# Optimization experiments

Hardware: AMD Instinct MI355X
Metric: run time of the kernel (lower is better)

The kernel has to match this reference:

```python
import jax, jax.numpy as jnp
import numpy as np
from jax import lax

N, K, F = 512, 512, 96
DM = 256   # hidden_dim == d_model
DS = 256   # d_state (must equal d_model for the original code to run)
L = 2      # num_layers
EPS = 1e-5


def layer_norm(x, g, b):
    mu = jnp.mean(x, axis=-1, keepdims=True)
    var = jnp.var(x, axis=-1, keepdims=True)
    return (x - mu) * jax.lax.rsqrt(var + EPS) * g + b


def setup_inputs() -> dict:
    key = jax.random.key(0)
    ks = jax.random.split(key, 20)
    n = lambda k, shape, s=0.02: jax.random.normal(k, shape, dtype=jnp.float32) * s
    inp = {
        "x": jax.random.normal(ks[0], (N, K, F), dtype=jnp.float32),
        # input_proj
        "in_w": n(ks[1], (DM, F), 0.05), "in_b": jnp.zeros((DM,), jnp.float32),
        "in_ln_g": jnp.ones((DM,), jnp.float32), "in_ln_b": jnp.zeros((DM,), jnp.float32),
        # per-layer Mamba params, stacked on leading L axis
        "ln_g": jnp.ones((L, DM), jnp.float32), "ln_b": jnp.zeros((L, DM), jnp.float32),
        "gate_w": n(ks[2], (L, DM, DM), 0.05), "gate_b": jnp.zeros((L, DM), jnp.float32),
        "sp_w": n(ks[3], (L, DS, DM), 0.05), "sp_b": jnp.zeros((L, DS), jnp.float32),
        "op_w": n(ks[4], (L, DM, DM), 0.05), "op_b": jnp.zeros((L, DM), jnp.float32),
        "A_log": n(ks[5], (L, DM, DS), 0.02),
        "D": jnp.ones((L, DM), jnp.float32),
        # output_proj
        "out_w": n(ks[6], (DM, DM), 0.05), "out_b": jnp.zeros((DM,), jnp.float32),
        "out_ln_g": jnp.ones((DM,), jnp.float32), "out_ln_b": jnp.zeros((DM,), jnp.float32),
    }
    return inp


def _ssm_scan(state0, decay, s):
    # state_t = decay * state_{t-1} + s_t ; s: [N, K, DS]
    def step(st, s_t):
        st = st * decay + s_t
        return st, st
    state, states = lax.scan(step, state0, jnp.swapaxes(s, 0, 1))
    return state, jnp.swapaxes(states, 0, 1)  # [N, K, DS]


def reference(x, in_w, in_b, in_ln_g, in_ln_b, ln_g, ln_b, gate_w, gate_b,
              sp_w, sp_b, op_w, op_b, A_log, D, out_w, out_b, out_ln_g, out_ln_b):
    # input_proj: Linear -> LayerNorm -> GELU
    h = jnp.einsum('nkf,df->nkd', x, in_w) + in_b
    h = jax.nn.gelu(layer_norm(h, in_ln_g, in_ln_b), approximate=False)

    state = jnp.zeros((x.shape[0], DS), dtype=h.dtype)
    for l in range(L):
        res = h
        z = layer_norm(h, ln_g[l], ln_b[l])
        xg = jax.nn.silu(jnp.einsum('nkd,ed->nke', z, gate_w[l]) + gate_b[l])
        s = jnp.einsum('nkd,sd->nks', xg, sp_w[l]) + sp_b[l]          # state_proj
        decay = jnp.exp(-jnp.mean(jnp.exp(A_log[l]), axis=-1))         # exp(mean(A)), A=-exp(A_log)
        state, states = _ssm_scan(state, decay, s)
        y = jnp.einsum('nks,sd->nkd', states, sp_w[l]) + D[l] * xg     # matmul(state, W_sp) + D*u
        h = jnp.einsum('nkd,ed->nke', y, op_w[l]) + op_b[l] + res      # out_proj + residual

    pooled = h[:, -1, :]                                               # pooling='last'
    out = jnp.einsum('nd,ed->ne', pooled, out_w) + out_b
    out = jax.nn.gelu(layer_norm(out, out_ln_g, out_ln_b), approximate=False)
    return out
```

## Files before the change

kernel.cpp:

```cpp
#include <hip/hip_runtime.h>
#include <hip/hip_bf16.h>


typedef __attribute__((ext_vector_type(8))) __bf16 bf16x8;
typedef __attribute__((ext_vector_type(8))) short short8;
typedef __attribute__((ext_vector_type(4))) float f32x4;
typedef __attribute__((ext_vector_type(4))) unsigned u32x4;

#define NSEQ 512
#define KSEQ 512
#define FIN 96
#define DMODEL 256
#define MTOT (NSEQ*KSEQ)

__device__ __forceinline__ unsigned short f2bf(float f){
  union { float f; unsigned u; } v; v.f = f;
  unsigned r = (v.u + 0x7FFFu + ((v.u >> 16) & 1u)) >> 16;
  return (unsigned short)r;
}
__device__ __forceinline__ float bf2f(unsigned short b){
  union { unsigned u; float f; } v; v.u = ((unsigned)b) << 16; return v.f;
}
__device__ __forceinline__ unsigned pk_bf16(float lo, float hi){
  unsigned r;
  asm("v_cvt_pk_bf16_f32 %0, %1, %2" : "=v"(r) : "v"(lo), "v"(hi));
  return r;
}
__device__ __forceinline__ float gelu_f(float x){
  return 0.5f * x * (1.0f + erff(x * 0.70710678118654752440f));
}
__device__ __forceinline__ float silu_f(float x){
  return x / (1.0f + __expf(-x));
}
__device__ __forceinline__ unsigned swzA(int row, int kbyte){
  return ((unsigned)(row*512 + kbyte)) ^ (unsigned)((row & 7) << 4);
}
__device__ __forceinline__ unsigned swzB(int n, int kbyte){
  return ((unsigned)(n*128 + kbyte)) ^ (unsigned)((n & 7) << 4);
}

__device__ __forceinline__ void gemm_w8(const unsigned short* __restrict__ wb,
                                        const char* As, f32x4 (&acc)[4][2],
                                        int lane, int c0)
{
  const int lr  = lane & 15;
  const int lk8 = (lane >> 4) * 8;
  const unsigned short* bp = wb + (size_t)(c0 + lr)*256 + lk8;
  bf16x8 bb[4][2];
  #pragma unroll
  for(int p = 0; p < 4; ++p)
    #pragma unroll
    for(int fc = 0; fc < 2; ++fc)
      bb[p][fc] = *(const bf16x8*)(bp + fc*4096 + p*32);
  #pragma unroll
  for(int kc = 0; kc < 8; ++kc){
    bf16x8 af[4];
    #pragma unroll
    for(int fr = 0; fr < 4; ++fr)
      af[fr] = *(const bf16x8*)(As + swzA(fr*16 + lr, kc*64 + lk8*2));
    #pragma unroll
    for(int fr = 0; fr < 4; ++fr)
      #pragma unroll
      for(int fc = 0; fc < 2; ++fc)
        acc[fr][fc] = __builtin_amdgcn_mfma_f32_16x16x32_bf16(af[fr], bb[kc&3][fc], acc[fr][fc], 0, 0, 0);
    if(kc < 4){
      #pragma unroll
      for(int fc = 0; fc < 2; ++fc)
        bb[kc&3][fc] = *(const bf16x8*)(bp + fc*4096 + (kc+4)*32);
    }
  }
}

__device__ __forceinline__ void zero_acc2(f32x4 (&acc)[4][2]){
  #pragma unroll
  for(int a=0;a<4;++a)
    #pragma unroll
    for(int b=0;b<2;++b)
      acc[a][b] = (f32x4){0.f,0.f,0.f,0.f};
}
__device__ __forceinline__ void zero_acc(f32x4 (&acc)[4][4]){
  #pragma unroll
  for(int a=0;a<4;++a)
    #pragma unroll
    for(int b=0;b<4;++b)
      acc[a][b] = (f32x4){0.f,0.f,0.f,0.f};
}

template<int KCH>
__device__ __forceinline__ void gemm_64x256(const unsigned short* __restrict__ wb,
                                            char* As, char* Bs,
                                            f32x4 (&acc)[4][4], int tid)
{
  const int lane = tid & 63;
  const int c0   = (tid >> 6) * 64;
  const int lr   = lane & 15;
  const int lk16 = (lane >> 4) * 16;
  #pragma unroll
  for(int kc = 0; kc < KCH; ++kc){
    __syncthreads();
    {
      const unsigned short* src = wb + (size_t)tid * (KCH*64) + kc*64;
      #pragma unroll
      for(int i = 0; i < 8; ++i){
        short8 v = *(const short8*)(src + i*8);
        *(short8*)(Bs + swzB(tid, i*16)) = v;
      }
    }
    __syncthreads();
    #pragma unroll
    for(int t2 = 0; t2 < 2; ++t2){
      bf16x8 af[4], bfr[4];
      #pragma unroll
      for(int fr = 0; fr < 4; ++fr)
        af[fr] = *(const bf16x8*)(As + swzA(fr*16 + lr, kc*128 + t2*64 + lk16));
      #pragma unroll
      for(int fc = 0; fc < 4; ++fc)
        bfr[fc] = *(const bf16x8*)(Bs + swzB(c0 + fc*16 + lr, t2*64 + lk16));
      #pragma unroll
      for(int fr = 0; fr < 4; ++fr)
        #pragma unroll
        for(int fc = 0; fc < 4; ++fc)
          acc[fr][fc] = __builtin_amdgcn_mfma_f32_16x16x32_bf16(af[fr], bfr[fc], acc[fr][fc], 0, 0, 0);
    }
  }
}

__global__ void k_cvt(const float* __restrict__ s, unsigned short* __restrict__ d, int n){
  int i = blockIdx.x*256 + threadIdx.x;
  if(i < n) d[i] = f2bf(s[i]);
}
__global__ void k_cvt_inw(const float* __restrict__ w, unsigned short* __restrict__ d){
  int i = blockIdx.x*256 + threadIdx.x;
  int n = i >> 7, f = i & 127;
  d[i] = (f < 96) ? f2bf(w[n*96 + f]) : (unsigned short)0;
}
__global__ void k_spT(const float* __restrict__ spw, unsigned short* __restrict__ d){
  int l = blockIdx.y;
  int i = blockIdx.x*256 + threadIdx.x;
  int dd = i >> 8, ss = i & 255;
  d[l*65536 + i] = f2bf(spw[l*65536 + ss*256 + dd]);
}
__global__ void k_decay(const float* __restrict__ A_log, float* __restrict__ decay){
  __shared__ float red[4];
  const int b = blockIdx.x;
  const int tid = threadIdx.x;
  float v = expf(A_log[(size_t)b*256 + tid]);
  #pragma unroll
  for(int o = 32; o >= 1; o >>= 1) v += __shfl_xor(v, o);
  if((tid & 63) == 0) red[tid >> 6] = v;
  __syncthreads();
  if(tid == 0){
    float s = red[0] + red[1] + red[2] + red[3];
    decay[b] = expf(-s * (1.f/256.f));
  }
}

__global__ __launch_bounds__(256) void k_in_proj(
    const float* __restrict__ x_g,
    const unsigned short* __restrict__ in_wb,
    const float* __restrict__ in_b,
    const float* __restrict__ ln_gv, const float* __restrict__ ln_bv,
    unsigned short* __restrict__ h_g)
{
  __shared__ char smem[65536];
  char* As = smem; char* Bs = smem + 32768;
  const int tid = threadIdx.x;
  const int m0 = blockIdx.x * 64;
  const int lane = tid & 63, c0w = (tid>>6)*64, lr = lane & 15, rb = (lane>>4)*4;
  {
    const int r = tid >> 2, cq = tid & 3;
    const float* src = x_g + (size_t)(m0 + r)*FIN + cq*24;
    unsigned short tmp[24] __attribute__((aligned(16)));
    #pragma unroll
    for(int i = 0; i < 6; ++i){
      float4 v = *(const float4*)(src + i*4);
      tmp[4*i]=f2bf(v.x); tmp[4*i+1]=f2bf(v.y); tmp[4*i+2]=f2bf(v.z); tmp[4*i+3]=f2bf(v.w);
    }
    #pragma unroll
    for(int i = 0; i < 3; ++i)
      *(short8*)(As + swzA(r, cq*48 + i*16)) = *(const short8*)(tmp + i*8);
    if(cq == 3){
      short8 z8 = {0,0,0,0,0,0,0,0};
      #pragma unroll
      for(int i = 0; i < 4; ++i)
        *(short8*)(As + swzA(r, 192 + i*16)) = z8;
    }
  }
  f32x4 acc[4][4]; zero_acc(acc);
  gemm_64x256<2>(in_wb, As, Bs, acc, tid);
  __syncthreads();
  #pragma unroll
  for(int fc = 0; fc < 4; ++fc){
    const int col = c0w + fc*16 + lr;
    const float bb = in_b[col];
    #pragma unroll
    for(int fr = 0; fr < 4; ++fr)
      #pragma unroll
      for(int rg = 0; rg < 4; ++rg){
        const int row = fr*16 + rb + rg;
        *(float*)(smem + (((unsigned)(row*1024 + col*4)) ^ ((row&7)<<4))) = acc[fr][fc][rg] + bb;
      }
  }
  __syncthreads();
  {
    const int r = tid >> 2, c0 = (tid & 3) * 64;
    float vals[64]; float sm = 0.f, sq = 0.f;
    #pragma unroll
    for(int i = 0; i < 16; ++i){
      float4 v = *(const float4*)(smem + (((unsigned)(r*1024 + (c0 + i*4)*4)) ^ ((r&7)<<4)));
      vals[4*i]=v.x; vals[4*i+1]=v.y; vals[4*i+2]=v.z; vals[4*i+3]=v.w;
    }
    #pragma unroll
    for(int i = 0; i < 64; ++i){ sm += vals[i]; sq += vals[i]*vals[i]; }
    sm += __shfl_xor(sm, 1); sm += __shfl_xor(sm, 2);
    sq += __shfl_xor(sq, 1); sq += __shfl_xor(sq, 2);
    const float mu = sm * (1.f/256.f);
    const float rstd = rsqrtf(sq * (1.f/256.f) - mu*mu + 1e-5f);
    unsigned short* dst = h_g + (size_t)(m0 + r)*DMODEL + c0;
    #pragma unroll
    for(int i = 0; i < 8; ++i){
      float g[8];
      #pragma unroll
      for(int j = 0; j < 8; ++j){
        const int c = c0 + i*8 + j;
        g[j] = gelu_f((vals[i*8+j]-mu)*rstd*ln_gv[c] + ln_bv[c]);
      }
      u32x4 o;
      o[0] = pk_bf16(g[0],g[1]); o[1] = pk_bf16(g[2],g[3]);
      o[2] = pk_bf16(g[4],g[5]); o[3] = pk_bf16(g[6],g[7]);
      *(u32x4*)(dst + i*8) = o;
    }
  }
}

__global__ __launch_bounds__(512,2) void k_layers(
    unsigned short* __restrict__ h_g,
    const unsigned short* __restrict__ gate_w0,
    const unsigned short* __restrict__ sp_w0,
    const unsigned short* __restrict__ spT_w0,
    const unsigned short* __restrict__ op_w0,
    const float* __restrict__ ln_g0, const float* __restrict__ ln_b0,
    const float* __restrict__ gate_b0, const float* __restrict__ sp_b0,
    const float* __restrict__ decay0, const float* __restrict__ D0,
    const float* __restrict__ op_b0)
{
  __shared__ char As[32768];
  __shared__ char Ss[32768];
  const int tid = threadIdx.x;
  const int n = blockIdx.x;
  const int lane = tid & 63;
  const int c0w = (tid >> 6) * 32;
  const int lr = lane & 15, rb = (lane>>4)*4;
  const int rA = tid >> 3, cAh = (tid & 7) * 32;
  float st = 0.f;

  #pragma unroll 1
  for(int l = 0; l < 2; ++l){
    const unsigned short* gw  = gate_w0 + l*65536;
    const unsigned short* spw = sp_w0   + l*65536;
    const unsigned short* spT = spT_w0  + l*65536;
    const unsigned short* opw = op_w0   + l*65536;
    const float* lg  = ln_g0   + l*256;
    const float* lb  = ln_b0   + l*256;
    const float* gb_ = gate_b0 + l*256;
    const float* sb_ = sp_b0   + l*256;
    const float* Dv_ = D0      + l*256;
    const float* ob_ = op_b0   + l*256;
    const float dc = decay0[l*256 + (tid & 255)];

    #pragma unroll 1
    for(int kb = 0; kb < 8; ++kb){
      const int m0 = n*KSEQ + kb*64;
      {
        const unsigned short* src = h_g + (size_t)(m0 + rA)*DMODEL + cAh;
        short8 hv[4];
        #pragma unroll
        for(int i = 0; i < 4; ++i) hv[i] = *(const short8*)(src + i*8);
        float sm = 0.f, sq = 0.f;
        #pragma unroll
        for(int i = 0; i < 4; ++i)
          #pragma unroll
          for(int j = 0; j < 8; ++j){
            float v = bf2f((unsigned short)hv[i][j]); sm += v; sq += v*v;
          }
        sm += __shfl_xor(sm, 1); sm += __shfl_xor(sm, 2); sm += __shfl_xor(sm, 4);
        sq += __shfl_xor(sq, 1); sq += __shfl_xor(sq, 2); sq += __shfl_xor(sq, 4);
        const float mu = sm * (1.f/256.f);
        const float rstd = rsqrtf(sq * (1.f/256.f) - mu*mu + 1e-5f);
        #pragma unroll
        for(int i = 0; i < 4; ++i){
          float z[8];
          #pragma unroll
          for(int j = 0; j < 8; ++j){
            const int c = cAh + i*8 + j;
            z[j] = (bf2f((unsigned short)hv[i][j])-mu)*rstd*lg[c] + lb[c];
          }
          u32x4 zz;
          zz[0] = pk_bf16(z[0],z[1]); zz[1] = pk_bf16(z[2],z[3]);
          zz[2] = pk_bf16(z[4],z[5]); zz[3] = pk_bf16(z[6],z[7]);
          *(u32x4*)(As + swzA(rA, cAh*2 + i*16)) = zz;
        }
      }
      __syncthreads();
      f32x4 acc[4][2]; zero_acc2(acc);
      gemm_w8(gw, As, acc, lane, c0w);
      #pragma unroll
      for(int fc = 0; fc < 2; ++fc){
        const int col = c0w + fc*16 + lr;
        const float gb = gb_[col];
        #pragma unroll
        for(int fr = 0; fr < 4; ++fr){
          const int row = fr*16 + rb;
          float v0 = silu_f(acc[fr][fc][0] + gb), v1 = silu_f(acc[fr][fc][1] + gb);
          float v2 = silu_f(acc[fr][fc][2] + gb), v3 = silu_f(acc[fr][fc][3] + gb);
          unsigned p0 = pk_bf16(v0, v1), p1 = pk_bf16(v2, v3);
          *(unsigned short*)(Ss + swzA(row+0, col*2)) = (unsigned short)p0;
          *(unsigned short*)(Ss + swzA(row+1, col*2)) = (unsigned short)(p0 >> 16);
          *(unsigned short*)(Ss + swzA(row+2, col*2)) = (unsigned short)p1;
          *(unsigned short*)(Ss + swzA(row+3, col*2)) = (unsigned short)(p1 >> 16);
        }
      }
      __syncthreads();
      zero_acc2(acc);
      gemm_w8(spw, Ss, acc, lane, c0w);
      #pragma unroll
      for(int fc = 0; fc < 2; ++fc){
        const int col = c0w + fc*16 + lr;
        const float sb = sb_[col];
        #pragma unroll
        for(int fr = 0; fr < 4; ++fr){
          const int row = fr*16 + rb;
          unsigned p0 = pk_bf16(acc[fr][fc][0] + sb, acc[fr][fc][1] + sb);
          unsigned p1 = pk_bf16(acc[fr][fc][2] + sb, acc[fr][fc][3] + sb);
          *(unsigned short*)(As + swzA(row+0, col*2)) = (unsigned short)p0;
          *(unsigned short*)(As + swzA(row+1, col*2)) = (unsigned short)(p0 >> 16);
          *(unsigned short*)(As + swzA(row+2, col*2)) = (unsigned short)p1;
          *(unsigned short*)(As + swzA(row+3, col*2)) = (unsigned short)(p1 >> 16);
        }
      }
      __syncthreads();
      if(tid < 256){
        #pragma unroll
        for(int c4 = 0; c4 < 4; ++c4){
          const int base = c4*16;
          float v[16];
          #pragma unroll
          for(int j = 0; j < 16; ++j)
            v[j] = bf2f(*(const unsigned short*)(As + swzA(base+j, tid*2)));
          #pragma unroll
          for(int j = 0; j < 16; ++j){ st = st*dc + v[j]; v[j] = st; }
          #pragma unroll
          for(int j = 0; j < 8; ++j){
            unsigned p = pk_bf16(v[2*j], v[2*j+1]);
            *(unsigned short*)(As + swzA(base+2*j,   tid*2)) = (unsigned short)p;
            *(unsigned short*)(As + swzA(base+2*j+1, tid*2)) = (unsigned short)(p >> 16);
          }
        }
      }
      __syncthreads();
      zero_acc2(acc);
      gemm_w8(spT, As, acc, lane, c0w);
      __syncthreads();
      #pragma unroll
      for(int fc = 0; fc < 2; ++fc){
        const int col = c0w + fc*16 + lr;
        const float Dv = Dv_[col];
        #pragma unroll
        for(int fr = 0; fr < 4; ++fr){
          const int row = fr*16 + rb;
          float y0 = acc[fr][fc][0] + Dv*bf2f(*(const unsigned short*)(Ss + swzA(row+0, col*2)));
          float y1 = acc[fr][fc][1] + Dv*bf2f(*(const unsigned short*)(Ss + swzA(row+1, col*2)));
          float y2 = acc[fr][fc][2] + Dv*bf2f(*(const unsigned short*)(Ss + swzA(row+2, col*2)));
          float y3 = acc[fr][fc][3] + Dv*bf2f(*(const unsigned short*)(Ss + swzA(row+3, col*2)));
          unsigned p0 = pk_bf16(y0, y1), p1 = pk_bf16(y2, y3);
          *(unsigned short*)(As + swzA(row+0, col*2)) = (unsigned short)p0;
          *(unsigned short*)(As + swzA(row+1, col*2)) = (unsigned short)(p0 >> 16);
          *(unsigned short*)(As + swzA(row+2, col*2)) = (unsigned short)p1;
          *(unsigned short*)(As + swzA(row+3, col*2)) = (unsigned short)(p1 >> 16);
        }
      }
      __syncthreads();
      zero_acc2(acc);
      gemm_w8(opw, As, acc, lane, c0w);
      #pragma unroll
      for(int fc = 0; fc < 2; ++fc){
        const int col = c0w + fc*16 + lr;
        const float ob = ob_[col];
        #pragma unroll
        for(int fr = 0; fr < 4; ++fr){
          const int row = fr*16 + rb;
          unsigned p0 = pk_bf16(acc[fr][fc][0] + ob, acc[fr][fc][1] + ob);
          unsigned p1 = pk_bf16(acc[fr][fc][2] + ob, acc[fr][fc][3] + ob);
          *(unsigned short*)(Ss + swzA(row+0, col*2)) = (unsigned short)p0;
          *(unsigned short*)(Ss + swzA(row+1, col*2)) = (unsigned short)(p0 >> 16);
          *(unsigned short*)(Ss + swzA(row+2, col*2)) = (unsigned short)p1;
          *(unsigned short*)(Ss + swzA(row+3, col*2)) = (unsigned short)(p1 >> 16);
        }
      }
      __syncthreads();
      {
        char* dst = (char*)(h_g + (size_t)m0*DMODEL);
        #pragma unroll
        for(int i = 0; i < 4; ++i){
          const unsigned flat = (unsigned)(i*8192 + tid*16);
          const unsigned row = flat >> 9;
          short8 a = *(const short8*)(Ss + (flat ^ ((row & 7u) << 4)));
          short8 hv = *(const short8*)(dst + flat);
          u32x4 o;
          #pragma unroll
          for(int j = 0; j < 4; ++j){
            float s0 = bf2f((unsigned short)a[2*j])   + bf2f((unsigned short)hv[2*j]);
            float s1 = bf2f((unsigned short)a[2*j+1]) + bf2f((unsigned short)hv[2*j+1]);
            o[j] = pk_bf16(s0, s1);
          }
          *(u32x4*)(dst + flat) = o;
        }
      }
    }
  }
}

__global__ __launch_bounds__(256) void k_out(
    const unsigned short* __restrict__ h_g,
    const unsigned short* __restrict__ out_wb,
    const float* __restrict__ out_bv,
    const float* __restrict__ ln_gv, const float* __restrict__ ln_bv,
    float* __restrict__ out_g)
{
  __shared__ char smem[65536];
  char* As = smem; char* Bs = smem + 32768;
  const int tid = threadIdx.x;
  const int r0 = blockIdx.x * 64;
  const int lane = tid & 63, c0w = (tid>>6)*64, lr = lane & 15, rb = (lane>>4)*4;
  {
    const int r = tid >> 2, c0 = (tid & 3) * 64;
    const unsigned short* src = h_g + ((size_t)(r0 + r)*KSEQ + (KSEQ-1))*DMODEL + c0;
    #pragma unroll
    for(int i = 0; i < 8; ++i){
      short8 v = *(const short8*)(src + i*8);
      *(short8*)(As + swzA(r, c0*2 + i*16)) = v;
    }
  }
  f32x4 acc[4][4]; zero_acc(acc);
  gemm_64x256<4>(out_wb, As, Bs, acc, tid);
  __syncthreads();
  #pragma unroll
  for(int fc = 0; fc < 4; ++fc){
    const int col = c0w + fc*16 + lr;
    const float bb = out_bv[col];
    #pragma unroll
    for(int fr = 0; fr < 4; ++fr)
      #pragma unroll
      for(int rg = 0; rg < 4; ++rg){
        const int row = fr*16 + rb + rg;
        *(float*)(smem + (((unsigned)(row*1024 + col*4)) ^ ((row&7)<<4))) = acc[fr][fc][rg] + bb;
      }
  }
  __syncthreads();
  {
    const int r = tid >> 2, c0 = (tid & 3) * 64;
    float vals[64]; float sm = 0.f, sq = 0.f;
    #pragma unroll
    for(int i = 0; i < 16; ++i){
      float4 v = *(const float4*)(smem + (((unsigned)(r*1024 + (c0 + i*4)*4)) ^ ((r&7)<<4)));
      vals[4*i]=v.x; vals[4*i+1]=v.y; vals[4*i+2]=v.z; vals[4*i+3]=v.w;
    }
    #pragma unroll
    for(int i = 0; i < 64; ++i){ sm += vals[i]; sq += vals[i]*vals[i]; }
    sm += __shfl_xor(sm, 1); sm += __shfl_xor(sm, 2);
    sq += __shfl_xor(sq, 1); sq += __shfl_xor(sq, 2);
    const float mu = sm * (1.f/256.f);
    const float rstd = rsqrtf(sq * (1.f/256.f) - mu*mu + 1e-5f);
    float* dst = out_g + (size_t)(r0 + r)*DMODEL + c0;
    #pragma unroll
    for(int i = 0; i < 16; ++i){
      float4 o;
      o.x = gelu_f((vals[4*i+0]-mu)*rstd*ln_gv[c0+i*4+0] + ln_bv[c0+i*4+0]);
      o.y = gelu_f((vals[4*i+1]-mu)*rstd*ln_gv[c0+i*4+1] + ln_bv[c0+i*4+1]);
      o.z = gelu_f((vals[4*i+2]-mu)*rstd*ln_gv[c0+i*4+2] + ln_bv[c0+i*4+2]);
      o.w = gelu_f((vals[4*i+3]-mu)*rstd*ln_gv[c0+i*4+3] + ln_bv[c0+i*4+3]);
      *(float4*)(dst + i*4) = o;
    }
  }
}

extern "C" void kernel_launch(void* const* d_in, const int* in_sizes, int n_in,
                              void* d_out, int out_size, void* d_ws, size_t ws_size,
                              hipStream_t stream) {
  (void)in_sizes; (void)n_in; (void)out_size; (void)ws_size;
  const float* x        = (const float*)d_in[0];
  const float* in_w     = (const float*)d_in[1];
  const float* in_b     = (const float*)d_in[2];
  const float* in_ln_g  = (const float*)d_in[3];
  const float* in_ln_b  = (const float*)d_in[4];
  const float* ln_g     = (const float*)d_in[5];
  const float* ln_b     = (const float*)d_in[6];
  const float* gate_w   = (const float*)d_in[7];
  const float* gate_b   = (const float*)d_in[8];
  const float* sp_w     = (const float*)d_in[9];
  const float* sp_b     = (const float*)d_in[10];
  const float* op_w     = (const float*)d_in[11];
  const float* op_b     = (const float*)d_in[12];
  const float* A_log    = (const float*)d_in[13];
  const float* Dp       = (const float*)d_in[14];
  const float* out_w    = (const float*)d_in[15];
  const float* out_b    = (const float*)d_in[16];
  const float* out_ln_g = (const float*)d_in[17];
  const float* out_ln_b = (const float*)d_in[18];

  char* ws = (char*)d_ws;
  unsigned short* h_g       = (unsigned short*)(ws + 0);
  float*          decay     = (float*)(ws + 134217728);
  unsigned short* wbase     = (unsigned short*)(ws + 134219776);
  unsigned short* in_wb  = wbase;
  unsigned short* gate_wb= in_wb  + 32768;
  unsigned short* sp_wb  = gate_wb+ 131072;
  unsigned short* sp_wTb = sp_wb  + 131072;
  unsigned short* op_wb  = sp_wTb + 131072;
  unsigned short* out_wb = op_wb  + 131072;

  k_cvt_inw<<<128, 256, 0, stream>>>(in_w, in_wb);
  k_cvt<<<512, 256, 0, stream>>>(gate_w, gate_wb, 131072);
  k_cvt<<<512, 256, 0, stream>>>(sp_w,   sp_wb,   131072);
  k_cvt<<<512, 256, 0, stream>>>(op_w,   op_wb,   131072);
  k_cvt<<<256, 256, 0, stream>>>(out_w,  out_wb,  65536);
  k_spT<<<dim3(256,2), 256, 0, stream>>>(sp_w, sp_wTb);
  k_decay<<<512, 256, 0, stream>>>(A_log, decay);

  k_in_proj<<<MTOT/64, 256, 0, stream>>>(x, in_wb, in_b, in_ln_g, in_ln_b, h_g);
  k_layers<<<NSEQ, 512, 0, stream>>>(h_g, gate_wb, sp_wb, sp_wTb, op_wb,
      ln_g, ln_b, gate_b, sp_b, decay, Dp, op_b);
  k_out<<<NSEQ/64, 256, 0, stream>>>(h_g, out_wb, out_b, out_ln_g, out_ln_b, (float*)d_out);
}
```

Before: 1.061 ms.

## Trim block barriers in fused Mamba layer loop and ping-pong LDS buffers

Replaces __syncthreads with a lighter barrier that waits only on LDS counters before s_barrier. It also removes two barriers by alternating which shared buffer (As/Ss) holds the y and out_proj results, and has each warp do the residual add on its own column slice. The block-wide residual pass that needed a barrier before it is gone, and one barrier is added at the end of the iteration. The catch is that correctness now depends on the LDS-only waitcnt and on each warp's residual rows and columns matching the columns it wrote; the per-warp residual access pattern also gives less coalesced global access to h.

```diff
diff --git a/kernel.cpp b/kernel.cpp
--- a/kernel.cpp
+++ b/kernel.cpp
@@ -31,6 +31,10 @@
 }
 __device__ __forceinline__ float silu_f(float x){
   return x / (1.0f + __expf(-x));
+}
+__device__ __forceinline__ void barx(){
+  asm volatile("s_waitcnt lgkmcnt(0)" ::: "memory");
+  __builtin_amdgcn_s_barrier();
 }
 __device__ __forceinline__ unsigned swzA(int row, int kbyte){
   return ((unsigned)(row*512 + kbyte)) ^ (unsigned)((row & 7) << 4);
@@ -301,7 +305,7 @@
           *(u32x4*)(As + swzA(rA, cAh*2 + i*16)) = zz;
         }
       }
-      __syncthreads();
+      barx();
       f32x4 acc[4][2]; zero_acc2(acc);
       gemm_w8(gw, As, acc, lane, c0w);
       #pragma unroll
@@ -320,7 +324,7 @@
           *(unsigned short*)(Ss + swzA(row+3, col*2)) = (unsigned short)(p1 >> 16);
         }
       }
-      __syncthreads();
+      barx();
       zero_acc2(acc);
       gemm_w8(spw, Ss, acc, lane, c0w);
       #pragma unroll
@@ -338,7 +342,7 @@
           *(unsigned short*)(As + swzA(row+3, col*2)) = (unsigned short)(p1 >> 16);
         }
       }
-      __syncthreads();
+      barx();
       if(tid < 256){
         #pragma unroll
         for(int c4 = 0; c4 < 4; ++c4){
@@ -357,10 +361,9 @@
           }
         }
       }
-      __syncthreads();
+      barx();
       zero_acc2(acc);
       gemm_w8(spT, As, acc, lane, c0w);
-      __syncthreads();
       #pragma unroll
       for(int fc = 0; fc < 2; ++fc){
         const int col = c0w + fc*16 + lr;
@@ -373,39 +376,40 @@
           float y2 = acc[fr][fc][2] + Dv*bf2f(*(const unsigned short*)(Ss + swzA(row+2, col*2)));
           float y3 = acc[fr][fc][3] + Dv*bf2f(*(const unsigned short*)(Ss + swzA(row+3, col*2)));
           unsigned p0 = pk_bf16(y0, y1), p1 = pk_bf16(y2, y3);
+          *(unsigned short*)(Ss + swzA(row+0, col*2)) = (unsigned short)p0;
+          *(unsigned short*)(Ss + swzA(row+1, col*2)) = (unsigned short)(p0 >> 16);
+          *(unsigned short*)(Ss + swzA(row+2, col*2)) = (unsigned short)p1;
+          *(unsigned short*)(Ss + swzA(row+3, col*2)) = (unsigned short)(p1 >> 16);
+        }
+      }
+      barx();
+      zero_acc2(acc);
+      gemm_w8(opw, Ss, acc, lane, c0w);
+      #pragma unroll
+      for(int fc = 0; fc < 2; ++fc){
+        const int col = c0w + fc*16 + lr;
+        const float ob = ob_[col];
+        #pragma unroll
+        for(int fr = 0; fr < 4; ++fr){
+          const int row = fr*16 + rb;
+          unsigned p0 = pk_bf16(acc[fr][fc][0] + ob, acc[fr][fc][1] + ob);
+          unsigned p1 = pk_bf16(acc[fr][fc][2] + ob, acc[fr][fc][3] + ob);
           *(unsigned short*)(As + swzA(row+0, col*2)) = (unsigned short)p0;
           *(unsigned short*)(As + swzA(row+1, col*2)) = (unsigned short)(p0 >> 16);
           *(unsigned short*)(As + swzA(row+2, col*2)) = (unsigned short)p1;
           *(unsigned short*)(As + swzA(row+3, col*2)) = (unsigned short)(p1 >> 16);
         }
       }
-      __syncthreads();
-      zero_acc2(acc);
-      gemm_w8(opw, As, acc, lane, c0w);
-      #pragma unroll
-      for(int fc = 0; fc < 2; ++fc){
-        const int col = c0w + fc*16 + lr;
-        const float ob = ob_[col];
-        #pragma unroll
-        for(int fr = 0; fr < 4; ++fr){
-          const int row = fr*16 + rb;
-          unsigned p0 = pk_bf16(acc[fr][fc][0] + ob, acc[fr][fc][1] + ob);
-          unsigned p1 = pk_bf16(acc[fr][fc][2] + ob, acc[fr][fc][3] + ob);
-          *(unsigned short*)(Ss + swzA(row+0, col*2)) = (unsigned short)p0;
-          *(unsigned short*)(Ss + swzA(row+1, col*2)) = (unsigned short)(p0 >> 16);
-          *(unsigned short*)(Ss + swzA(row+2, col*2)) = (unsigned short)p1;
-          *(unsigned short*)(Ss + swzA(row+3, col*2)) = (unsigned short)(p1 >> 16);
-        }
-      }
-      __syncthreads();
       {
-        char* dst = (char*)(h_g + (size_t)m0*DMODEL);
-        #pragma unroll
-        for(int i = 0; i < 4; ++i){
-          const unsigned flat = (unsigned)(i*8192 + tid*16);
-          const unsigned row = flat >> 9;
-          short8 a = *(const short8*)(Ss + (flat ^ ((row & 7u) << 4)));
-          short8 hv = *(const short8*)(dst + flat);
+        char* hb = (char*)(h_g + (size_t)m0*DMODEL);
+        const int cl = lane & 3;
+        const int rbase = lane >> 2;
+        #pragma unroll
+        for(int p = 0; p < 4; ++p){
+          const int row = p*16 + rbase;
+          const unsigned gof = (unsigned)(row*512 + c0w*2 + cl*16);
+          short8 a = *(const short8*)(As + swzA(row, c0w*2 + cl*16));
+          short8 hv = *(const short8*)(hb + gof);
           u32x4 o;
           #pragma unroll
           for(int j = 0; j < 4; ++j){
@@ -413,9 +417,10 @@
             float s1 = bf2f((unsigned short)a[2*j+1]) + bf2f((unsigned short)hv[2*j+1]);
             o[j] = pk_bf16(s0, s1);
           }
-          *(u32x4*)(dst + flat) = o;
-        }
-      }
+          *(u32x4*)(hb + gof) = o;
+        }
+      }
+      barx();
     }
   }
 }
```

Result: slower. 1.100 ms (+3.7%).
